# Kernel optimization log

Hardware: AMD Instinct MI355X
Metric: run time of the kernel (lower is better)

The kernel has to match this reference:

```python
import jax, jax.numpy as jnp
import numpy as np

H = 12          # num heads
D = 768         # hidden size
DH = D // H     # size per head
FF = 3072       # intermediate size
EPS = 1e-11


def gelu(x):
    # tanh approximation, matching the TF source exactly
    c = np.sqrt(2.0 / np.pi).astype(np.float32)
    return x * 0.5 * (1.0 + jnp.tanh(c * (x + 0.044715 * jnp.power(x, 3))))


def layer_norm(x, gamma, beta):
    mean = jnp.mean(x, axis=-1, keepdims=True)
    var = jnp.mean(jnp.square(x - mean), axis=-1, keepdims=True)
    return (x - mean) * jax.lax.rsqrt(var + EPS) * gamma + beta


def setup_inputs() -> dict:
    key = jax.random.key(0)
    ks = jax.random.split(key, 12)
    B, S = 16, 512
    std = 0.02
    inp = {
        "x": jax.random.normal(ks[0], (B, S, D), jnp.float32),
        "mask": jnp.ones((B, S), dtype=bool),
        "Wq": jax.random.normal(ks[1], (D, D), jnp.float32) * std,
        "bq": jnp.zeros((D,), jnp.float32),
        "Wk": jax.random.normal(ks[2], (D, D), jnp.float32) * std,
        "bk": jnp.zeros((D,), jnp.float32),
        "Wv": jax.random.normal(ks[3], (D, D), jnp.float32) * std,
        "bv": jnp.zeros((D,), jnp.float32),
        "Wo": jax.random.normal(ks[4], (D, D), jnp.float32) * std,
        "bo": jnp.zeros((D,), jnp.float32),
        "g1": jnp.ones((D,), jnp.float32),
        "b1": jnp.zeros((D,), jnp.float32),
        "Wi": jax.random.normal(ks[5], (D, FF), jnp.float32) * std,
        "bi": jnp.zeros((FF,), jnp.float32),
        "Wo2": jax.random.normal(ks[6], (FF, D), jnp.float32) * std,
        "bo2": jnp.zeros((D,), jnp.float32),
        "g2": jnp.ones((D,), jnp.float32),
        "b2": jnp.zeros((D,), jnp.float32),
    }
    return inp


def reference(x, mask, Wq, bq, Wk, bk, Wv, bv, Wo, bo, g1, b1, Wi, bi, Wo2, bo2, g2, b2):
    B, S, _ = x.shape
    # QKV projections
    q = (x @ Wq + bq).reshape(B, S, H, DH)
    k = (x @ Wk + bk).reshape(B, S, H, DH)
    v = (x @ Wv + bv).reshape(B, S, H, DH)
    # scaled dot-product attention scores [B, H, S, S]
    scores = jnp.einsum("bqhd,bkhd->bhqk", q, k) / np.sqrt(DH).astype(np.float32)
    # key-side mask, applied as score * m + (1 - m) * -100 (per original source)
    m = mask[:, None, None, :].astype(jnp.float32)
    scores = scores * m + (1.0 - m) * (-100.0)
    probs = jax.nn.softmax(scores, axis=-1)
    attn = jnp.einsum("bhqk,bkhd->bqhd", probs, v).reshape(B, S, D)
    # tf.boolean_mask with all-True mask -> flatten batch and seq dims
    attn = attn.reshape(B * S, D)
    x_flat = x.reshape(B * S, D)
    # attention output projection + residual + LN
    attn_out = layer_norm(attn @ Wo + bo + x_flat, g1, b1)
    # FFN: gelu dense then output dense + residual + LN
    inter = gelu(attn_out @ Wi + bi)
    out = layer_norm(inter @ Wo2 + bo2 + attn_out, g2, b2)
    return out
```

## Files before the change

### kernel.cpp

```cpp
#include <hip/hip_runtime.h>


#define DEV __device__ __forceinline__

typedef unsigned short u16;
typedef unsigned int   u32;
typedef __bf16 bf16x8 __attribute__((ext_vector_type(8)));
typedef float  f32x4  __attribute__((ext_vector_type(4)));
typedef unsigned short u16x8 __attribute__((ext_vector_type(8)));
typedef unsigned short u16x4 __attribute__((ext_vector_type(4)));

DEV u16 f2bf(float f) {
    u32 u = __builtin_bit_cast(u32, f);
    u += 0x7fffu + ((u >> 16) & 1u);
    return (u16)(u >> 16);
}

DEV float gelu_f(float x) {
    float u = 0.7978845608028654f * (x + 0.044715f * x * x * x);
    float e = __expf(2.f * u);
    return 0.5f * x * (2.f - 2.f / (e + 1.f));
}

DEV void gload16(const void* gsrc, void* ldst) {
    __builtin_amdgcn_global_load_lds(
        (__attribute__((address_space(1))) void*)(void*)(const_cast<void*>(gsrc)),
        (__attribute__((address_space(3))) void*)ldst, 16, 0, 0);
}

DEV f32x4 MFMA(bf16x8 a, bf16x8 b, f32x4 c) {
    return __builtin_amdgcn_mfma_f32_16x16x32_bf16(a, b, c, 0, 0, 0);
}

__global__ __launch_bounds__(256) void cvt_bf16(const float* __restrict__ in,
                                                u16* __restrict__ out, int n) {
    int i = (blockIdx.x * 256 + threadIdx.x) * 4;
    if (i >= n) return;
    f32x4 v = *(const f32x4*)(in + i);
    u16x4 o;
    o.x = f2bf(v.x); o.y = f2bf(v.y); o.z = f2bf(v.z); o.w = f2bf(v.w);
    *(u16x4*)(out + i) = o;
}

__global__ __launch_bounds__(256) void transpose_cvt(const float* __restrict__ in,
                                                     u16* __restrict__ out,
                                                     int R, int C) {
    __shared__ float tile[32][33];
    int tx = threadIdx.x & 31, ty = threadIdx.x >> 5;
    int r0 = blockIdx.y * 32, c0 = blockIdx.x * 32;
#pragma unroll
    for (int i = 0; i < 4; i++)
        tile[ty + i * 8][tx] = in[(size_t)(r0 + ty + i * 8) * C + c0 + tx];
    __syncthreads();
#pragma unroll
    for (int i = 0; i < 4; i++)
        out[(size_t)(c0 + ty + i * 8) * R + r0 + tx] = f2bf(tile[tx][ty + i * 8]);
}

__global__ void concat_bias(const float* __restrict__ bq, const float* __restrict__ bk,
                            const float* __restrict__ bv, float* __restrict__ o) {
    int i = blockIdx.x * 256 + threadIdx.x;
    if (i < 2304) o[i] = (i < 768) ? bq[i] : (i < 1536 ? bk[i - 768] : bv[i - 1536]);
}

template <int EPI>
__global__ __launch_bounds__(256) void gemm_bt(const u16* __restrict__ A,
                                               const u16* __restrict__ BT,
                                               const float* __restrict__ bias,
                                               void* __restrict__ Cout,
                                               int N, int K, int ntn) {
    __shared__ __align__(16) char smem[65536];
    const int t = threadIdx.x, lane = t & 63, wid = t >> 6;
    const int nwg = gridDim.x, bid = blockIdx.x;
    const int swz = ((nwg & 7) == 0) ? ((bid & 7) * (nwg >> 3) + (bid >> 3)) : bid;
    const int tm = swz / ntn, tn = swz % ntn;
    const int wm = wid >> 1, wn = wid & 1;

    f32x4 acc[4][4];
#pragma unroll
    for (int i = 0; i < 4; i++)
#pragma unroll
        for (int j = 0; j < 4; j++) acc[i][j] = f32x4{0.f, 0.f, 0.f, 0.f};

    const u16* Ab = A + (size_t)tm * 128 * K;
    const u16* Bb = BT + (size_t)tn * 128 * K;
    const int so = lane * 16;
    const int srin = so >> 7;
    const int scol = ((so & 127) ^ ((srin & 7) << 4)) >> 1;

#define STG(KT, BUF)                                                          \
    {                                                                         \
        char* As_ = smem + (BUF) * 32768;                                     \
        char* Bs_ = As_ + 16384;                                              \
        _Pragma("unroll")                                                     \
        for (int i_ = 0; i_ < 4; i_++) {                                      \
            int cw_ = wid * 4 + i_;                                           \
            int row_ = cw_ * 8 + srin;                                        \
            gload16(Ab + (size_t)row_ * K + (KT) + scol, As_ + cw_ * 1024);   \
            gload16(Bb + (size_t)row_ * K + (KT) + scol, Bs_ + cw_ * 1024);   \
        }                                                                     \
    }

    const int NT = K >> 6;
    STG(0, 0);
    __syncthreads();

    for (int k = 0; k < NT; ++k) {
        if (k + 1 < NT) STG((k + 1) << 6, (k & 1) ^ 1);
        const char* As = smem + (k & 1) * 32768;
        const char* Bs = As + 16384;
#pragma unroll
        for (int ks = 0; ks < 2; ++ks) {
            bf16x8 af[4], bfr[4];
#pragma unroll
            for (int mi = 0; mi < 4; mi++) {
                int row = wm * 64 + mi * 16 + (lane & 15);
                int cb = (ks * 64 + ((lane >> 4) << 4)) ^ ((row & 7) << 4);
                af[mi] = *(const bf16x8*)(As + row * 128 + cb);
            }
#pragma unroll
            for (int ni = 0; ni < 4; ni++) {
                int row = wn * 64 + ni * 16 + (lane & 15);
                int cb = (ks * 64 + ((lane >> 4) << 4)) ^ ((row & 7) << 4);
                bfr[ni] = *(const bf16x8*)(Bs + row * 128 + cb);
            }
            __builtin_amdgcn_s_setprio(1);
#pragma unroll
            for (int mi = 0; mi < 4; mi++)
#pragma unroll
                for (int ni = 0; ni < 4; ni++)
                    acc[mi][ni] = MFMA(af[mi], bfr[ni], acc[mi][ni]);
            __builtin_amdgcn_s_setprio(0);
        }
        __syncthreads();
    }
#undef STG

    const int r0 = tm * 128 + wm * 64, c0 = tn * 128 + wn * 64;
    float bcol[4];
#pragma unroll
    for (int ni = 0; ni < 4; ni++) bcol[ni] = bias[c0 + ni * 16 + (lane & 15)];
#pragma unroll
    for (int mi = 0; mi < 4; mi++) {
#pragma unroll
        for (int r = 0; r < 4; r++) {
            int gr = r0 + mi * 16 + ((lane >> 4) << 2) + r;
#pragma unroll
            for (int ni = 0; ni < 4; ni++) {
                int gc = c0 + ni * 16 + (lane & 15);
                float v = acc[mi][ni][r] + bcol[ni];
                if constexpr (EPI == 2) v = gelu_f(v);
                if constexpr (EPI == 1)
                    ((float*)Cout)[(size_t)gr * N + gc] = v;
                else
                    ((u16*)Cout)[(size_t)gr * N + gc] = f2bf(v);
            }
        }
    }
}

__global__ __launch_bounds__(256) void attn_kernel(const u16* __restrict__ QKV,
                                                   u16* __restrict__ attnb) {
    __shared__ __align__(16) char sm[24576];
    char* Ks = sm;
    char* Vt = sm + 8192;
    const int t = threadIdx.x, lane = t & 63, wid = t >> 6;
    const int qt = blockIdx.x, bh = blockIdx.y;
    const int b = bh / 12, h = bh % 12;
    const size_t base = (size_t)b * 512 * 2304;
    char* Pw = sm + 16384 + wid * 2048;

    bf16x8 aq[2];
    {
        int qrow = qt * 64 + wid * 16 + (lane & 15);
        const u16* qp = QKV + base + (size_t)qrow * 2304 + h * 64 + ((lane >> 4) << 3);
        aq[0] = *(const bf16x8*)qp;
        aq[1] = *(const bf16x8*)(qp + 32);
    }
    f32x4 oacc[4];
#pragma unroll
    for (int g = 0; g < 4; g++) oacc[g] = f32x4{0.f, 0.f, 0.f, 0.f};
    float mrun[4] = {-1e30f, -1e30f, -1e30f, -1e30f};
    float lrun[4] = {0.f, 0.f, 0.f, 0.f};

    for (int kt = 0; kt < 8; ++kt) {
        __syncthreads();
#pragma unroll
        for (int i = 0; i < 2; i++) {
            int cw = wid * 2 + i;
            int o = cw * 1024 + lane * 16;
            int row = o >> 7;
            int cb = (o & 127) ^ ((row & 7) << 4);
            gload16(QKV + base + (size_t)(kt * 64 + row) * 2304 + 768 + h * 64 + (cb >> 1),
                    Ks + cw * 1024);
        }
        {
            int key = t & 63, dh0 = wid * 16;
            const u16* vp = QKV + base + (size_t)(kt * 64 + key) * 2304 + 1536 + h * 64 + dh0;
            u16x8 v0 = *(const u16x8*)vp;
            u16x8 v1 = *(const u16x8*)(vp + 8);
#pragma unroll
            for (int j = 0; j < 8; j++) {
                int dh = dh0 + j;
                *(u16*)(Vt + dh * 128 + ((key * 2) ^ ((dh & 7) << 4))) = v0[j];
            }
#pragma unroll
            for (int j = 0; j < 8; j++) {
                int dh = dh0 + 8 + j;
                *(u16*)(Vt + dh * 128 + ((key * 2) ^ ((dh & 7) << 4))) = v1[j];
            }
        }
        __syncthreads();

        f32x4 sacc[4];
#pragma unroll
        for (int ni = 0; ni < 4; ni++) sacc[ni] = f32x4{0.f, 0.f, 0.f, 0.f};
#pragma unroll
        for (int ni = 0; ni < 4; ni++) {
            int row = ni * 16 + (lane & 15);
#pragma unroll
            for (int ks = 0; ks < 2; ks++) {
                int cb = (ks * 64 + ((lane >> 4) << 4)) ^ ((row & 7) << 4);
                bf16x8 bk = *(const bf16x8*)(Ks + row * 128 + cb);
                sacc[ni] = MFMA(aq[ks], bk, sacc[ni]);
            }
        }
#pragma unroll
        for (int ni = 0; ni < 4; ni++)
#pragma unroll
            for (int r = 0; r < 4; r++) sacc[ni][r] *= 0.125f;

#pragma unroll
        for (int r = 0; r < 4; r++) {
            float pm = fmaxf(fmaxf(sacc[0][r], sacc[1][r]), fmaxf(sacc[2][r], sacc[3][r]));
            pm = fmaxf(pm, __shfl_xor(pm, 1));
            pm = fmaxf(pm, __shfl_xor(pm, 2));
            pm = fmaxf(pm, __shfl_xor(pm, 4));
            pm = fmaxf(pm, __shfl_xor(pm, 8));
            float mnew = fmaxf(mrun[r], pm);
            float sf = __expf(mrun[r] - mnew);
            mrun[r] = mnew;
            lrun[r] *= sf;
#pragma unroll
            for (int g = 0; g < 4; g++) oacc[g][r] *= sf;
            int prow = ((lane >> 4) << 2) + r;
            float ps = 0.f;
#pragma unroll
            for (int ni = 0; ni < 4; ni++) {
                float p = __expf(sacc[ni][r] - mnew);
                ps += p;
                int col = ni * 16 + (lane & 15);
                *(u16*)(Pw + prow * 128 + ((col * 2) ^ ((prow & 7) << 4))) = f2bf(p);
            }
            ps += __shfl_xor(ps, 1);
            ps += __shfl_xor(ps, 2);
            ps += __shfl_xor(ps, 4);
            ps += __shfl_xor(ps, 8);
            lrun[r] += ps;
        }
        __syncthreads();

#pragma unroll
        for (int ks = 0; ks < 2; ks++) {
            int prow = lane & 15;
            int pcb = (ks * 64 + ((lane >> 4) << 4)) ^ ((prow & 7) << 4);
            bf16x8 ap = *(const bf16x8*)(Pw + prow * 128 + pcb);
#pragma unroll
            for (int g = 0; g < 4; g++) {
                int vrow = g * 16 + (lane & 15);
                int vcb = (ks * 64 + ((lane >> 4) << 4)) ^ ((vrow & 7) << 4);
                bf16x8 bv = *(const bf16x8*)(Vt + vrow * 128 + vcb);
                oacc[g] = MFMA(ap, bv, oacc[g]);
            }
        }
    }

#pragma unroll
    for (int g = 0; g < 4; g++)
#pragma unroll
        for (int r = 0; r < 4; r++) {
            int qrow = qt * 64 + wid * 16 + ((lane >> 4) << 2) + r;
            float o = oacc[g][r] / lrun[r];
            attnb[(size_t)(b * 512 + qrow) * 768 + h * 64 + g * 16 + (lane & 15)] = f2bf(o);
        }
}

__global__ __launch_bounds__(256) void ln_kernel(const float* __restrict__ Y,
                                                 const float* __restrict__ res,
                                                 const float* __restrict__ g,
                                                 const float* __restrict__ bta,
                                                 float* __restrict__ outf,
                                                 u16* __restrict__ outb) {
    int row = blockIdx.x, t = threadIdx.x, lane = t & 63, wid = t >> 6;
    const float* y = Y + (size_t)row * 768;
    const float* rr = res + (size_t)row * 768;
    float v[3];
#pragma unroll
    for (int i = 0; i < 3; i++) v[i] = y[t + i * 256] + rr[t + i * 256];

    float s = v[0] + v[1] + v[2];
#pragma unroll
    for (int o = 32; o; o >>= 1) s += __shfl_xor(s, o);
    __shared__ float sm[4];
    __shared__ float bc[2];
    if (lane == 0) sm[wid] = s;
    __syncthreads();
    if (t == 0) bc[0] = (sm[0] + sm[1] + sm[2] + sm[3]) * (1.f / 768.f);
    __syncthreads();
    float mean = bc[0];

    float q = 0.f;
#pragma unroll
    for (int i = 0; i < 3; i++) { float d = v[i] - mean; q += d * d; }
#pragma unroll
    for (int o = 32; o; o >>= 1) q += __shfl_xor(q, o);
    if (lane == 0) sm[wid] = q;
    __syncthreads();
    if (t == 0) bc[1] = rsqrtf((sm[0] + sm[1] + sm[2] + sm[3]) * (1.f / 768.f) + 1e-11f);
    __syncthreads();
    float rs = bc[1];
#pragma unroll
    for (int i = 0; i < 3; i++) {
        int c = t + i * 256;
        float o = (v[i] - mean) * rs * g[c] + bta[c];
        outf[(size_t)row * 768 + c] = o;
        if (outb) outb[(size_t)row * 768 + c] = f2bf(o);
    }
}

extern "C" void kernel_launch(void* const* d_in, const int* in_sizes, int n_in,
                              void* d_out, int out_size, void* d_ws, size_t ws_size,
                              hipStream_t stream) {
    const float* x   = (const float*)d_in[0];
    const float* Wq  = (const float*)d_in[2];
    const float* bq  = (const float*)d_in[3];
    const float* Wk  = (const float*)d_in[4];
    const float* bk  = (const float*)d_in[5];
    const float* Wv  = (const float*)d_in[6];
    const float* bv  = (const float*)d_in[7];
    const float* Wo  = (const float*)d_in[8];
    const float* bo  = (const float*)d_in[9];
    const float* g1  = (const float*)d_in[10];
    const float* b1  = (const float*)d_in[11];
    const float* Wi  = (const float*)d_in[12];
    const float* bi  = (const float*)d_in[13];
    const float* Wo2 = (const float*)d_in[14];
    const float* bo2 = (const float*)d_in[15];
    const float* g2  = (const float*)d_in[16];
    const float* b2  = (const float*)d_in[17];

    char* w = (char*)d_ws;
    size_t off = 0;
    auto alloc = [&](size_t n) { size_t o = off; off += (n + 255) & ~(size_t)255; return o; };
    size_t oXb    = alloc((size_t)8192 * 768 * 2);
    size_t oWqkvT = alloc((size_t)2304 * 768 * 2);
    size_t oWoT   = alloc((size_t)768 * 768 * 2);
    size_t oWiT   = alloc((size_t)3072 * 768 * 2);
    size_t oWo2T  = alloc((size_t)768 * 3072 * 2);
    size_t oBqkv  = alloc((size_t)2304 * 4);
    size_t oR0    = alloc((size_t)8192 * 3072 * 2);
    size_t oY     = alloc((size_t)8192 * 768 * 4);
    size_t oAof   = alloc((size_t)8192 * 768 * 4);
    size_t oAob   = alloc((size_t)8192 * 768 * 2);
    (void)ws_size; (void)in_sizes; (void)n_in; (void)out_size;

    u16*   Xb    = (u16*)(w + oXb);
    u16*   WqkvT = (u16*)(w + oWqkvT);
    u16*   WoT   = (u16*)(w + oWoT);
    u16*   WiT   = (u16*)(w + oWiT);
    u16*   Wo2T  = (u16*)(w + oWo2T);
    float* bqkv  = (float*)(w + oBqkv);
    u16*   QKV   = (u16*)(w + oR0);
    u16*   attnb = (u16*)(w + oR0 + (size_t)8192 * 2304 * 2);
    u16*   inter = (u16*)(w + oR0);
    float* Y     = (float*)(w + oY);
    float* aof   = (float*)(w + oAof);
    u16*   aob   = (u16*)(w + oAob);

    cvt_bf16<<<6144, 256, 0, stream>>>(x, Xb, 8192 * 768);
    transpose_cvt<<<dim3(24, 24), 256, 0, stream>>>(Wq, WqkvT, 768, 768);
    transpose_cvt<<<dim3(24, 24), 256, 0, stream>>>(Wk, WqkvT + 768 * 768, 768, 768);
    transpose_cvt<<<dim3(24, 24), 256, 0, stream>>>(Wv, WqkvT + 2 * 768 * 768, 768, 768);
    transpose_cvt<<<dim3(24, 24), 256, 0, stream>>>(Wo, WoT, 768, 768);
    transpose_cvt<<<dim3(96, 24), 256, 0, stream>>>(Wi, WiT, 768, 3072);
    transpose_cvt<<<dim3(24, 96), 256, 0, stream>>>(Wo2, Wo2T, 3072, 768);
    concat_bias<<<9, 256, 0, stream>>>(bq, bk, bv, bqkv);

    gemm_bt<0><<<1152, 256, 0, stream>>>(Xb, WqkvT, bqkv, QKV, 2304, 768, 18);
    attn_kernel<<<dim3(8, 192), 256, 0, stream>>>(QKV, attnb);
    gemm_bt<1><<<384, 256, 0, stream>>>(attnb, WoT, bo, Y, 768, 768, 6);
    ln_kernel<<<8192, 256, 0, stream>>>(Y, x, g1, b1, aof, aob);
    gemm_bt<2><<<1536, 256, 0, stream>>>(aob, WiT, bi, inter, 3072, 768, 24);
    gemm_bt<1><<<384, 256, 0, stream>>>(inter, Wo2T, bo2, Y, 768, 3072, 6);
    ln_kernel<<<8192, 256, 0, stream>>>(Y, aof, g2, b2, (float*)d_out, nullptr);
}
```

Before: 281.1 us.

## Add 4-stage pipelined BK=32 GEMM variant for QKV and FFN1 with 2-wave occupancy

Adds a new GEMM body for the QKV and FFN1 projections. It uses a 32-wide K step, a four-buffer LDS ring with loads issued three steps ahead, counted vmcnt waits, one barrier per step, and raised wave priority around the MFMA block. The kernels are marked for two workgroups per CU so load latency can overlap better. The Wo and FFN2 GEMMs keep the old body through thin wrappers. The risk is more barriers per unit of work and register pressure under the occupancy bound.

```diff
diff --git a/kernel.cpp b/kernel.cpp
--- a/kernel.cpp
+++ b/kernel.cpp
@@ -64,11 +64,126 @@
 }
 
 template <int EPI>
-__global__ __launch_bounds__(256) void gemm_bt(const u16* __restrict__ A,
-                                               const u16* __restrict__ BT,
-                                               const float* __restrict__ bias,
-                                               void* __restrict__ Cout,
-                                               int N, int K, int ntn) {
+DEV void gemm_q_body(const u16* __restrict__ A, const u16* __restrict__ BT,
+                     const float* __restrict__ bias, void* __restrict__ Cout,
+                     int N, int K, int ntn) {
+    __shared__ __align__(16) char smem[65536];
+    const int t = threadIdx.x, lane = t & 63, wid = t >> 6;
+    const int nwg = gridDim.x, bid = blockIdx.x;
+    const int swzb = ((nwg & 7) == 0) ? ((bid & 7) * (nwg >> 3) + (bid >> 3)) : bid;
+    const int tm = swzb / ntn, tn = swzb % ntn;
+    const int wm = wid >> 1, wn = wid & 1;
+
+    f32x4 acc[4][4];
+#pragma unroll
+    for (int i = 0; i < 4; i++)
+#pragma unroll
+        for (int j = 0; j < 4; j++) acc[i][j] = f32x4{0.f, 0.f, 0.f, 0.f};
+
+    const int NT = K >> 5;
+    const u16* Ab = A + (size_t)tm * 128 * K;
+    const u16* Bb = BT + (size_t)tn * 128 * K;
+
+    int sr[2], sc[2];
+#pragma unroll
+    for (int j = 0; j < 2; j++) {
+        int X = t * 16 + j * 4096;
+        int row = X >> 6;
+        int cb = (X & 63) ^ ((row & 3) << 4);
+        sr[j] = row; sc[j] = cb >> 1;
+    }
+    const u16* pA0 = Ab + (size_t)sr[0] * K + sc[0];
+    const u16* pA1 = Ab + (size_t)sr[1] * K + sc[1];
+    const u16* pB0 = Bb + (size_t)sr[0] * K + sc[0];
+    const u16* pB1 = Bb + (size_t)sr[1] * K + sc[1];
+    const int dA0 = wid * 1024, dA1 = wid * 1024 + 4096;
+
+    const int g16 = (lane >> 4) << 4, swz = (lane & 3) << 4;
+    const int aoff = ((wm * 64 + (lane & 15)) * 64 + g16) ^ swz;
+    const int boff = 8192 + (((wn * 64 + (lane & 15)) * 64 + g16) ^ swz);
+
+#define STGQ(TT)                                                       \
+    {                                                                  \
+        char* b_ = smem + ((TT) & 3) * 16384;                          \
+        int ko_ = (TT) * 32;                                           \
+        gload16(pA0 + ko_, b_ + dA0);                                  \
+        gload16(pA1 + ko_, b_ + dA1);                                  \
+        gload16(pB0 + ko_, b_ + 8192 + dA0);                           \
+        gload16(pB1 + ko_, b_ + 8192 + dA1);                           \
+    }
+
+    STGQ(0) STGQ(1) STGQ(2)
+    asm volatile("s_waitcnt vmcnt(8)" ::: "memory");
+    __builtin_amdgcn_s_barrier();
+    __builtin_amdgcn_sched_barrier(0);
+    asm volatile("" ::: "memory");
+
+    for (int tt = 0; tt < NT; ++tt) {
+        const char* buf = smem + (tt & 3) * 16384;
+        if (tt + 3 < NT) STGQ(tt + 3)
+        bf16x8 af[4], bfr[4];
+#pragma unroll
+        for (int mi = 0; mi < 4; mi++) af[mi] = *(const bf16x8*)(buf + aoff + mi * 1024);
+#pragma unroll
+        for (int ni = 0; ni < 4; ni++) bfr[ni] = *(const bf16x8*)(buf + boff + ni * 1024);
+        __builtin_amdgcn_s_setprio(1);
+#pragma unroll
+        for (int mi = 0; mi < 4; mi++)
+#pragma unroll
+            for (int ni = 0; ni < 4; ni++)
+                acc[mi][ni] = MFMA(af[mi], bfr[ni], acc[mi][ni]);
+        __builtin_amdgcn_s_setprio(0);
+        if (tt + 1 < NT) {
+            int ahead = NT - 2 - tt; ahead = ahead > 2 ? 2 : (ahead < 0 ? 0 : ahead);
+            if (ahead == 2)      asm volatile("s_waitcnt vmcnt(8)" ::: "memory");
+            else if (ahead == 1) asm volatile("s_waitcnt vmcnt(4)" ::: "memory");
+            else                 asm volatile("s_waitcnt vmcnt(0)" ::: "memory");
+        }
+        __builtin_amdgcn_s_barrier();
+        __builtin_amdgcn_sched_barrier(0);
+        asm volatile("" ::: "memory");
+    }
+#undef STGQ
+
+    const int r0 = tm * 128 + wm * 64, c0 = tn * 128 + wn * 64;
+    float cb[4];
+#pragma unroll
+    for (int ni = 0; ni < 4; ni++) cb[ni] = bias[c0 + ni * 16 + (lane & 15)];
+#pragma unroll
+    for (int mi = 0; mi < 4; mi++) {
+#pragma unroll
+        for (int r = 0; r < 4; r++) {
+            int gr = r0 + mi * 16 + ((lane >> 4) << 2) + r;
+#pragma unroll
+            for (int ni = 0; ni < 4; ni++) {
+                int gc = c0 + ni * 16 + (lane & 15);
+                float v = acc[mi][ni][r] + cb[ni];
+                if constexpr (EPI == 2) v = gelu_f(v);
+                ((u16*)Cout)[(size_t)gr * N + gc] = f2bf(v);
+            }
+        }
+    }
+}
+
+__global__ __launch_bounds__(256, 2) void gemm_qkv(const u16* __restrict__ A,
+                                                   const u16* __restrict__ BT,
+                                                   const float* __restrict__ bias,
+                                                   void* __restrict__ Cout,
+                                                   int N, int K, int ntn) {
+    gemm_q_body<0>(A, BT, bias, Cout, N, K, ntn);
+}
+__global__ __launch_bounds__(256, 2) void gemm_ffn1(const u16* __restrict__ A,
+                                                    const u16* __restrict__ BT,
+                                                    const float* __restrict__ bias,
+                                                    void* __restrict__ Cout,
+                                                    int N, int K, int ntn) {
+    gemm_q_body<2>(A, BT, bias, Cout, N, K, ntn);
+}
+
+template <int EPI>
+DEV void gemm_bt_body(const u16* __restrict__ A, const u16* __restrict__ BT,
+                      const float* __restrict__ bias, void* __restrict__ Cout,
+                      int N, int K, int ntn) {
     __shared__ __align__(16) char smem[65536];
     const int t = threadIdx.x, lane = t & 63, wid = t >> 6;
     const int nwg = gridDim.x, bid = blockIdx.x;
@@ -157,6 +272,21 @@
             }
         }
     }
+}
+
+__global__ __launch_bounds__(256) void gemm_wo(const u16* __restrict__ A,
+                                               const u16* __restrict__ BT,
+                                               const float* __restrict__ bias,
+                                               void* __restrict__ Cout,
+                                               int N, int K, int ntn) {
+    gemm_bt_body<1>(A, BT, bias, Cout, N, K, ntn);
+}
+__global__ __launch_bounds__(256) void gemm_ffn2(const u16* __restrict__ A,
+                                                 const u16* __restrict__ BT,
+                                                 const float* __restrict__ bias,
+                                                 void* __restrict__ Cout,
+                                                 int N, int K, int ntn) {
+    gemm_bt_body<1>(A, BT, bias, Cout, N, K, ntn);
 }
 
 __global__ __launch_bounds__(256) void attn_kernel(const u16* __restrict__ QKV,
@@ -386,11 +516,11 @@
     transpose_cvt<<<dim3(24, 96), 256, 0, stream>>>(Wo2, Wo2T, 3072, 768);
     concat_bias<<<9, 256, 0, stream>>>(bq, bk, bv, bqkv);
 
-    gemm_bt<0><<<1152, 256, 0, stream>>>(Xb, WqkvT, bqkv, QKV, 2304, 768, 18);
+    gemm_qkv<<<1152, 256, 0, stream>>>(Xb, WqkvT, bqkv, QKV, 2304, 768, 18);
     attn_kernel<<<dim3(8, 192), 256, 0, stream>>>(QKV, attnb);
-    gemm_bt<1><<<384, 256, 0, stream>>>(attnb, WoT, bo, Y, 768, 768, 6);
+    gemm_wo<<<384, 256, 0, stream>>>(attnb, WoT, bo, Y, 768, 768, 6);
     ln_kernel<<<8192, 256, 0, stream>>>(Y, x, g1, b1, aof, aob);
-    gemm_bt<2><<<1536, 256, 0, stream>>>(aob, WiT, bi, inter, 3072, 768, 24);
-    gemm_bt<1><<<384, 256, 0, stream>>>(inter, Wo2T, bo2, Y, 768, 3072, 6);
+    gemm_ffn1<<<1536, 256, 0, stream>>>(aob, WiT, bi, inter, 3072, 768, 24);
+    gemm_ffn2<<<384, 256, 0, stream>>>(inter, Wo2T, bo2, Y, 768, 3072, 6);
     ln_kernel<<<8192, 256, 0, stream>>>(Y, aof, g2, b2, (float*)d_out, nullptr);
 }
```

Measured after the change: 282.8 us. Within noise of the previous version (+0.6%).

## Load GEMM B operand straight to registers and halve shared memory per block

Applied to the files above, without the earlier changes.

The GEMM body now stages only the A tile through double-buffered shared memory. Each wave loads its B fragments directly from global memory into registers every k-step. Shared memory per block drops from 64KB to 32KB, and the kernels are split into separate wrappers with launch bounds requesting 3 blocks per CU, to raise occupancy and cut LDS traffic. The cost is that B fragments are now read from global/L2 twice per block (once by each wm wave pair) with no prefetch ahead of use, so memory latency may be exposed in the MFMA loop.

```diff
diff --git a/kernel.cpp b/kernel.cpp
--- a/kernel.cpp
+++ b/kernel.cpp
@@ -64,16 +64,14 @@
 }
 
 template <int EPI>
-__global__ __launch_bounds__(256) void gemm_bt(const u16* __restrict__ A,
-                                               const u16* __restrict__ BT,
-                                               const float* __restrict__ bias,
-                                               void* __restrict__ Cout,
-                                               int N, int K, int ntn) {
-    __shared__ __align__(16) char smem[65536];
+DEV void gemm_breg_body(const u16* __restrict__ A, const u16* __restrict__ BT,
+                        const float* __restrict__ bias, void* __restrict__ Cout,
+                        int N, int K, int ntn) {
+    __shared__ __align__(16) char smem[32768];
     const int t = threadIdx.x, lane = t & 63, wid = t >> 6;
     const int nwg = gridDim.x, bid = blockIdx.x;
-    const int swz = ((nwg & 7) == 0) ? ((bid & 7) * (nwg >> 3) + (bid >> 3)) : bid;
-    const int tm = swz / ntn, tn = swz % ntn;
+    const int swzb = ((nwg & 7) == 0) ? ((bid & 7) * (nwg >> 3) + (bid >> 3)) : bid;
+    const int tm = swzb / ntn, tn = swzb % ntn;
     const int wm = wid >> 1, wn = wid & 1;
 
     f32x4 acc[4][4];
@@ -82,59 +80,59 @@
 #pragma unroll
         for (int j = 0; j < 4; j++) acc[i][j] = f32x4{0.f, 0.f, 0.f, 0.f};
 
+    const int NT = K >> 6;
     const u16* Ab = A + (size_t)tm * 128 * K;
-    const u16* Bb = BT + (size_t)tn * 128 * K;
+    const u16* Bb = BT + (size_t)(tn * 128 + wn * 64 + (lane & 15)) * K
+                       + ((lane >> 4) << 3);
+
     const int so = lane * 16;
     const int srin = so >> 7;
     const int scol = ((so & 127) ^ ((srin & 7) << 4)) >> 1;
 
-#define STG(KT, BUF)                                                          \
+#define STGA(KT, BUF)                                                         \
     {                                                                         \
-        char* As_ = smem + (BUF) * 32768;                                     \
-        char* Bs_ = As_ + 16384;                                              \
+        char* As_ = smem + (BUF) * 16384;                                     \
         _Pragma("unroll")                                                     \
         for (int i_ = 0; i_ < 4; i_++) {                                      \
             int cw_ = wid * 4 + i_;                                           \
             int row_ = cw_ * 8 + srin;                                        \
             gload16(Ab + (size_t)row_ * K + (KT) + scol, As_ + cw_ * 1024);   \
-            gload16(Bb + (size_t)row_ * K + (KT) + scol, Bs_ + cw_ * 1024);   \
         }                                                                     \
     }
 
-    const int NT = K >> 6;
-    STG(0, 0);
-    __syncthreads();
-
-    for (int k = 0; k < NT; ++k) {
-        if (k + 1 < NT) STG((k + 1) << 6, (k & 1) ^ 1);
-        const char* As = smem + (k & 1) * 32768;
-        const char* Bs = As + 16384;
+    STGA(0, 0);
+    __syncthreads();
+
+    const int g16 = (lane >> 4) << 4;
+    for (int kt = 0; kt < NT; ++kt) {
+        if (kt + 1 < NT) STGA((kt + 1) << 6, (kt & 1) ^ 1);
+        const char* As = smem + (kt & 1) * 16384;
+        bf16x8 b0[4], b1[4];
+        const u16* bp = Bb + (size_t)kt * 64;
+#pragma unroll
+        for (int ni = 0; ni < 4; ni++) b0[ni] = *(const bf16x8*)(bp + (size_t)(ni * 16) * K);
+#pragma unroll
+        for (int ni = 0; ni < 4; ni++) b1[ni] = *(const bf16x8*)(bp + (size_t)(ni * 16) * K + 32);
 #pragma unroll
         for (int ks = 0; ks < 2; ++ks) {
-            bf16x8 af[4], bfr[4];
+            bf16x8 af[4];
 #pragma unroll
             for (int mi = 0; mi < 4; mi++) {
                 int row = wm * 64 + mi * 16 + (lane & 15);
-                int cb = (ks * 64 + ((lane >> 4) << 4)) ^ ((row & 7) << 4);
+                int cb = (ks * 64 + g16) ^ ((row & 7) << 4);
                 af[mi] = *(const bf16x8*)(As + row * 128 + cb);
             }
-#pragma unroll
-            for (int ni = 0; ni < 4; ni++) {
-                int row = wn * 64 + ni * 16 + (lane & 15);
-                int cb = (ks * 64 + ((lane >> 4) << 4)) ^ ((row & 7) << 4);
-                bfr[ni] = *(const bf16x8*)(Bs + row * 128 + cb);
-            }
             __builtin_amdgcn_s_setprio(1);
 #pragma unroll
             for (int mi = 0; mi < 4; mi++)
 #pragma unroll
                 for (int ni = 0; ni < 4; ni++)
-                    acc[mi][ni] = MFMA(af[mi], bfr[ni], acc[mi][ni]);
+                    acc[mi][ni] = MFMA(af[mi], (ks ? b1 : b0)[ni], acc[mi][ni]);
             __builtin_amdgcn_s_setprio(0);
         }
         __syncthreads();
     }
-#undef STG
+#undef STGA
 
     const int r0 = tm * 128 + wm * 64, c0 = tn * 128 + wn * 64;
     float bcol[4];
@@ -157,6 +155,35 @@
             }
         }
     }
+}
+
+__global__ __launch_bounds__(256, 3) void gemm_qkv(const u16* __restrict__ A,
+                                                   const u16* __restrict__ BT,
+                                                   const float* __restrict__ bias,
+                                                   void* __restrict__ Cout,
+                                                   int N, int K, int ntn) {
+    gemm_breg_body<0>(A, BT, bias, Cout, N, K, ntn);
+}
+__global__ __launch_bounds__(256, 3) void gemm_wo(const u16* __restrict__ A,
+                                                  const u16* __restrict__ BT,
+                                                  const float* __restrict__ bias,
+                                                  void* __restrict__ Cout,
+                                                  int N, int K, int ntn) {
+    gemm_breg_body<1>(A, BT, bias, Cout, N, K, ntn);
+}
+__global__ __launch_bounds__(256, 3) void gemm_ffn1(const u16* __restrict__ A,
+                                                    const u16* __restrict__ BT,
+                                                    const float* __restrict__ bias,
+                                                    void* __restrict__ Cout,
+                                                    int N, int K, int ntn) {
+    gemm_breg_body<2>(A, BT, bias, Cout, N, K, ntn);
+}
+__global__ __launch_bounds__(256, 3) void gemm_ffn2(const u16* __restrict__ A,
+                                                    const u16* __restrict__ BT,
+                                                    const float* __restrict__ bias,
+                                                    void* __restrict__ Cout,
+                                                    int N, int K, int ntn) {
+    gemm_breg_body<1>(A, BT, bias, Cout, N, K, ntn);
 }
 
 __global__ __launch_bounds__(256) void attn_kernel(const u16* __restrict__ QKV,
@@ -386,11 +413,11 @@
     transpose_cvt<<<dim3(24, 96), 256, 0, stream>>>(Wo2, Wo2T, 3072, 768);
     concat_bias<<<9, 256, 0, stream>>>(bq, bk, bv, bqkv);
 
-    gemm_bt<0><<<1152, 256, 0, stream>>>(Xb, WqkvT, bqkv, QKV, 2304, 768, 18);
+    gemm_qkv<<<1152, 256, 0, stream>>>(Xb, WqkvT, bqkv, QKV, 2304, 768, 18);
     attn_kernel<<<dim3(8, 192), 256, 0, stream>>>(QKV, attnb);
-    gemm_bt<1><<<384, 256, 0, stream>>>(attnb, WoT, bo, Y, 768, 768, 6);
+    gemm_wo<<<384, 256, 0, stream>>>(attnb, WoT, bo, Y, 768, 768, 6);
     ln_kernel<<<8192, 256, 0, stream>>>(Y, x, g1, b1, aof, aob);
-    gemm_bt<2><<<1536, 256, 0, stream>>>(aob, WiT, bi, inter, 3072, 768, 24);
-    gemm_bt<1><<<384, 256, 0, stream>>>(inter, Wo2T, bo2, Y, 768, 3072, 6);
+    gemm_ffn1<<<1536, 256, 0, stream>>>(aob, WiT, bi, inter, 3072, 768, 24);
+    gemm_ffn2<<<384, 256, 0, stream>>>(inter, Wo2T, bo2, Y, 768, 3072, 6);
     ln_kernel<<<8192, 256, 0, stream>>>(Y, aof, g2, b2, (float*)d_out, nullptr);
 }
```

New measurement: 407.0 us. 1.45x slower.
